# Kernel tuning notes

Measured on AMD Instinct MI355X. Metric: run time of the kernel, lower is better.

Reference implementation:

```python
import jax, jax.numpy as jnp
import numpy as np

B, E, H, L = 16, 64, 8, 2048   # batch, channels(in_channels), heads(node), seq_len
MODES = 64                     # min(modes, L//2) with 'lowest' selection
IDX_Q = np.arange(MODES)       # index_q = sorted(range(modes))
IDX_KV = np.arange(MODES)      # index_kv = sorted(range(modes))


def setup_inputs() -> dict:
    key = jax.random.key(0)
    kq, kk, kv, kr, ki = jax.random.split(key, 5)
    scale = 1.0 / (E * E)  # 1/(in_channels*out_channels)
    return {
        "q": jax.random.normal(kq, (B, E, H, L), jnp.float32),
        "k": jax.random.normal(kk, (B, E, H, L), jnp.float32),
        "v": jax.random.normal(kv, (B, E, H, L), jnp.float32),
        # complex weights1 stored as (real, imag) float parts; torch.rand(cfloat)
        # draws uniform[0,1) real and imag independently, scaled by `scale`.
        "w_re": scale * jax.random.uniform(kr, (H, E, E, MODES), jnp.float32),
        "w_im": scale * jax.random.uniform(ki, (H, E, E, MODES), jnp.float32),
    }


def reference(q, k, v, w_re, w_im):
    # q,k,v: [B,E,H,L] -> [B,H,E,L]; note v is NOT used (matches original module)
    xq = jnp.transpose(q, (0, 2, 1, 3))
    xk = jnp.transpose(k, (0, 2, 1, 3))

    # rFFT along time, gather selected frequency modes: [B,H,E,MODES] complex
    xq_ft_ = jnp.fft.rfft(xq, axis=-1)[..., IDX_Q]
    xk_ft_ = jnp.fft.rfft(xk, axis=-1)[..., IDX_KV]

    # complex cross-attention in mode space: [B,H,MODES,MODES]
    xqk_ft = jnp.einsum('bhex,bhey->bhxy', xq_ft_, xk_ft_)
    xqk_ft = jnp.tanh(xqk_ft)  # complex tanh, matching torch's tensor.tanh()

    # attend over kv modes (values == xk_ft_): [B,H,E,MODES]
    xqkv_ft = jnp.einsum('bhxy,bhey->bhex', xqk_ft, xk_ft_)

    # per-head complex channel mixing: [B,H,E,MODES]
    W = w_re + 1j * w_im  # [H,E,E,MODES]
    xqkvw = jnp.einsum('bhex,heox->bhox', xqkv_ft, W)

    # scatter back into full spectrum and invert
    out_ft = jnp.zeros((B, H, E, L // 2 + 1), jnp.complex64).at[..., IDX_Q].set(xqkvw)
    out = jnp.fft.irfft(out_ft / (E * E), n=L, axis=-1)  # [B,H,E,L] real
    return jnp.transpose(out, (0, 2, 1, 3))  # [B,E,H,L]
```

## Files before the change

kernel.cpp:

```cpp
#include <hip/hip_runtime.h>
#include <math.h>

#define B 16
#define E 64
#define H 8
#define L 2048
#define M 64
#define PLANE (B*H*E*M)

constexpr float CS32[32] = {
     1.0f,                    0.9807852804032304f,   0.9238795325112868f,   0.8314696123025452f,
     0.7071067811865476f,     0.5555702330196022f,   0.3826834323650898f,   0.1950903220161283f,
     0.0f,                   -0.1950903220161283f,  -0.3826834323650898f,  -0.5555702330196022f,
    -0.7071067811865476f,    -0.8314696123025452f,  -0.9238795325112868f,  -0.9807852804032304f,
    -1.0f,                   -0.9807852804032304f,  -0.9238795325112868f,  -0.8314696123025452f,
    -0.7071067811865476f,    -0.5555702330196022f,  -0.3826834323650898f,  -0.1950903220161283f,
     0.0f,                    0.1950903220161283f,   0.3826834323650898f,   0.5555702330196022f,
     0.7071067811865476f,     0.8314696123025452f,   0.9238795325112868f,   0.9807852804032304f
};
constexpr float SN32[32] = {
     0.0f,                    0.1950903220161283f,   0.3826834323650898f,   0.5555702330196022f,
     0.7071067811865476f,     0.8314696123025452f,   0.9238795325112868f,   0.9807852804032304f,
     1.0f,                    0.9807852804032304f,   0.9238795325112868f,   0.8314696123025452f,
     0.7071067811865476f,     0.5555702330196022f,   0.3826834323650898f,   0.1950903220161283f,
     0.0f,                   -0.1950903220161283f,  -0.3826834323650898f,  -0.5555702330196022f,
    -0.7071067811865476f,    -0.8314696123025452f,  -0.9238795325112868f,  -0.9807852804032304f,
    -1.0f,                   -0.9807852804032304f,  -0.9238795325112868f,  -0.8314696123025452f,
    -0.7071067811865476f,    -0.5555702330196022f,  -0.3826834323650898f,  -0.1950903220161283f
};

__device__ inline void ctanhf_stable(float x, float y, float& re, float& im) {
    float ax = fabsf(x);
    if (ax > 11.0f) { re = copysignf(1.0f, x); im = 0.0f; return; }
    float t    = tanf(y);
    float beta = 1.0f + t * t;
    float s    = sinhf(x);
    float rho  = sqrtf(1.0f + s * s);
    float den  = 1.0f + beta * s * s;
    re = (beta * rho * s) / den;
    im = t / den;
}

__global__ __launch_bounds__(256) void k_wtrans(const float* __restrict__ wre,
                                                const float* __restrict__ wim,
                                                float2* __restrict__ Wt,
                                                float2* __restrict__ Tgo,
                                                float2* __restrict__ Cgo)
{
    __shared__ float tre[64][65], tim[64][65];
    int h  = blockIdx.x >> 6, rt = blockIdx.x & 63;
    int tid = threadIdx.x;

    int gidx = blockIdx.x * 256 + tid;
    if (gidx < 2048) {
        int r = gidx >> 6, m = gidx & 63;
        double a = -3.14159265358979323846 * (double)(m * r) / 1024.0;
        Tgo[gidx] = make_float2((float)cos(a), (float)sin(a));
    } else if (gidx < 2080) {
        int j = gidx - 2048;
        double a = -3.14159265358979323846 * (double)j / 32.0;
        Cgo[j] = make_float2((float)cos(a), (float)sin(a));
    }

    int x = tid & 63, r4 = tid >> 6;
    const size_t base = ((size_t)h * 4096 + (size_t)rt * 64) * 64;
    #pragma unroll
    for (int j = 0; j < 16; ++j) {
        int row = j * 4 + r4;
        tre[row][x] = wre[base + (size_t)row * 64 + x];
        tim[row][x] = wim[base + (size_t)row * 64 + x];
    }
    __syncthreads();

    int row = tid & 63, x4 = tid >> 6;
    #pragma unroll
    for (int j = 0; j < 16; ++j) {
        int xx = j * 4 + x4;
        Wt[((size_t)h * 64 + xx) * 4096 + (size_t)rt * 64 + row] =
            make_float2(tre[row][xx], tim[row][xx]);
    }
}

__global__ __launch_bounds__(256) void k_dft(const float* __restrict__ q,
                                             const float* __restrict__ k,
                                             const float2* __restrict__ Tg,
                                             const float2* __restrict__ Cgl,
                                             float2* __restrict__ Xq,
                                             float2* __restrict__ Xk)
{
    __shared__ float2 Ysh[4][64][17];
    __shared__ float2 Tsm[32][64];
    __shared__ float2 Cgs[32];

    int tid  = threadIdx.x;
    int rloc = tid >> 6;
    int lane = tid & 63;
    int rid  = blockIdx.x * 4 + rloc;
    int tensor = rid >> 13;
    int r8 = rid & 8191;
    int b = r8 >> 9, h = (r8 >> 6) & 7, e = r8 & 63;

    #pragma unroll
    for (int j = 0; j < 8; ++j) ((float2*)Tsm)[tid + 256 * j] = Tg[tid + 256 * j];
    if (tid < 32) Cgs[tid] = Cgl[tid];
    __syncthreads();

    const float* src = (tensor ? k : q) + (((size_t)(b * E + e) * H + h) * L) + lane;
    float xs[32];
    #pragma unroll
    for (int i = 0; i < 32; ++i) xs[i] = src[i * 64];

    float s_[16], d_[16];
    #pragma unroll
    for (int i = 1; i <= 15; ++i) { s_[i] = xs[i] + xs[32 - i]; d_[i] = xs[i] - xs[32 - i]; }

    #pragma unroll
    for (int f = 0; f <= 16; ++f) {
        float ar = xs[0] + ((f & 1) ? -xs[16] : xs[16]);
        float ai = 0.f;
        #pragma unroll
        for (int i = 1; i <= 15; ++i) {
            ar = fmaf(s_[i], CS32[(f * i) & 31], ar);
            ai = fmaf(d_[i], SN32[(f * i) & 31], ai);
        }
        Ysh[rloc][lane][f] = make_float2(ar, -ai);
    }

    int mlow = lane & 31;
    int half = lane >> 5;
    int fi   = (mlow <= 16) ? mlow : 32 - mlow;
    float sgn = (mlow <= 16) ? 1.f : -1.f;

    float ar0 = 0.f, ai0 = 0.f, ar1 = 0.f, ai1 = 0.f;
    int rbase = half * 32;
    #pragma unroll
    for (int rb = 0; rb < 4; ++rb) {
        float2 tb[8], t2[8], yb[8];
        #pragma unroll
        for (int j = 0; j < 8; ++j) {
            int rp = rb * 8 + j;
            tb[j] = Tsm[rp][mlow];
            t2[j] = Tsm[rp][mlow + 32];
            yb[j] = Ysh[rloc][rbase + rp][fi];
        }
        #pragma unroll
        for (int j = 0; j < 8; ++j) {
            float yr = yb[j].x, yi = sgn * yb[j].y;
            ar0 = fmaf(yr, tb[j].x, ar0); ar0 = fmaf(-yi, tb[j].y, ar0);
            ai0 = fmaf(yr, tb[j].y, ai0); ai0 = fmaf(yi, tb[j].x, ai0);
            ar1 = fmaf(yr, t2[j].x, ar1); ar1 = fmaf(-yi, t2[j].y, ar1);
            ai1 = fmaf(yr, t2[j].y, ai1); ai1 = fmaf(yi, t2[j].x, ai1);
        }
    }

    if (half) {
        float2 c = Cgs[mlow];
        float t;
        t   = ar0 * c.x - ai0 * c.y;
        ai0 = ar0 * c.y + ai0 * c.x;  ar0 = t;
        t   = ar1 * c.x - ai1 * c.y;
        ai1 = ar1 * c.y + ai1 * c.x;  ar1 = t;
        ar1 = -ar1; ai1 = -ai1;
    }
    ar0 += __shfl_xor(ar0, 32);  ai0 += __shfl_xor(ai0, 32);
    ar1 += __shfl_xor(ar1, 32);  ai1 += __shfl_xor(ai1, 32);

    float2* dst = (tensor ? Xk : Xq) + ((size_t)(b * H + h) * E + e) * M;
    if (!half) dst[mlow]      = make_float2(ar0, ai0);
    else       dst[mlow + 32] = make_float2(ar1, ai1);
}

__global__ __launch_bounds__(256) void k_mid(const float2* __restrict__ Xq,
                                             const float2* __restrict__ Xk,
                                             float2* __restrict__ U)
{
    __shared__ float Qre[64][16], Qim[64][16];
    __shared__ float Kre[64][65], Kim[64][65];

    int bh = blockIdx.x >> 2;
    int xh = (blockIdx.x & 3) * 16;
    int b  = bh >> 3, h = bh & 7;
    int tid = threadIdx.x;
    const float2* xq = Xq + (size_t)bh * 4096;
    const float2* xk = Xk + (size_t)bh * 4096;

    #pragma unroll
    for (int j = 0; j < 4; ++j) {
        int idx = tid + 256 * j;
        int e = idx >> 4, xl = idx & 15;
        float2 v = xq[(e << 6) + xh + xl];
        Qre[e][xl] = v.x; Qim[e][xl] = v.y;
    }
    #pragma unroll
    for (int j = 0; j < 16; ++j) {
        int idx = tid + 256 * j;
        int e = idx >> 6, mm = idx & 63;
        float2 v = xk[idx];
        Kre[e][mm] = v.x; Kim[e][mm] = v.y;
    }
    __syncthreads();

    int x  = tid & 15;
    int y0 = (tid >> 4) * 4;
    float ar[4], ai[4];
    #pragma unroll
    for (int j = 0; j < 4; ++j) { ar[j] = 0.f; ai[j] = 0.f; }

    for (int e = 0; e < 64; ++e) {
        float qr = Qre[e][x], qi = Qim[e][x];
        #pragma unroll
        for (int j = 0; j < 4; ++j) {
            float kr = Kre[e][y0 + j], ki = Kim[e][y0 + j];
            ar[j] = fmaf(qr, kr, ar[j]); ar[j] = fmaf(-qi, ki, ar[j]);
            ai[j] = fmaf(qr, ki, ai[j]); ai[j] = fmaf( qi, kr, ai[j]);
        }
    }
    float trj[4], tij[4];
    #pragma unroll
    for (int j = 0; j < 4; ++j) ctanhf_stable(ar[j], ai[j], trj[j], tij[j]);

    __syncthreads();
    #pragma unroll
    for (int j = 0; j < 4; ++j) { Qre[y0 + j][x] = trj[j]; Qim[y0 + j][x] = tij[j]; }
    __syncthreads();

    int eL    = tid & 63;
    int xslot = tid >> 6;
    float ur[4], ui[4];
    #pragma unroll
    for (int j = 0; j < 4; ++j) { ur[j] = 0.f; ui[j] = 0.f; }

    for (int y = 0; y < 64; ++y) {
        float kr = Kre[eL][y], ki = Kim[eL][y];
        #pragma unroll
        for (int xp = 0; xp < 4; ++xp) {
            int xx = xp * 4 + xslot;
            float sr = Qre[y][xx], si = Qim[y][xx];
            ur[xp] += sr * kr - si * ki;
            ui[xp] += sr * ki + si * kr;
        }
    }
    #pragma unroll
    for (int xp = 0; xp < 4; ++xp) {
        int xx = xp * 4 + xslot;
        U[(((size_t)h * 64 + xh + xx) * 16 + b) * 64 + eL] = make_float2(ur[xp], ui[xp]);
    }
}

__global__ __launch_bounds__(256) void k_wmix(const float2* __restrict__ U,
                                              const float2* __restrict__ Wt,
                                              float2* __restrict__ R)
{
    __shared__ float2 Usm[16][64];
    __shared__ float2 Wsm[64][64];

    int h = blockIdx.x >> 6, x = blockIdx.x & 63;
    int tid = threadIdx.x;

    const float2* usrc = U  + ((size_t)h * 64 + x) * 1024;
    #pragma unroll
    for (int j = 0; j < 4; ++j) {
        int idx = tid + 256 * j;
        ((float2*)Usm)[idx] = usrc[idx];
    }
    const float2* wsrc = Wt + ((size_t)h * 64 + x) * 4096;
    #pragma unroll
    for (int j = 0; j < 16; ++j) {
        int idx = tid + 256 * j;
        ((float2*)Wsm)[idx] = wsrc[idx];
    }
    __syncthreads();

    int o = tid & 63, b0 = tid >> 6;
    float rr[4], ri[4];
    #pragma unroll
    for (int j = 0; j < 4; ++j) { rr[j] = 0.f; ri[j] = 0.f; }

    for (int e = 0; e < 64; ++e) {
        float2 w = Wsm[e][o];
        #pragma unroll
        for (int j = 0; j < 4; ++j) {
            float2 u = Usm[b0 + 4 * j][e];
            rr[j] += u.x * w.x - u.y * w.y;
            ri[j] += u.x * w.y + u.y * w.x;
        }
    }
    #pragma unroll
    for (int j = 0; j < 4; ++j) {
        int b = b0 + 4 * j;
        R[((size_t)(b * H + h) * 64 + o) * 64 + x] = make_float2(rr[j], ri[j]);
    }
}

__global__ __launch_bounds__(256) void k_irfft(const float2* __restrict__ R,
                                               float* __restrict__ out)
{
    __shared__ float2 Fsh[4][64];
    int rloc = threadIdx.x >> 6;
    int r    = threadIdx.x & 63;
    int bho  = blockIdx.x * 4 + rloc;
    int o  = bho & 63, bh = bho >> 6;
    int h  = bh & 7,   b  = bh >> 3;

    Fsh[rloc][r] = R[(size_t)bho * 64 + r];

    float sr_, cr_;
    sincosf(3.0679615757712823e-3f * (float)r, &sr_, &cr_);
    float s32, c32;
    sincosf(9.8174770424681038e-2f * (float)r, &s32, &c32);

    float gr[32], gi[32];
    float wr = 1.f, wi = 0.f;
    #pragma unroll
    for (int f = 0; f < 32; ++f) {
        float2 Fa = Fsh[rloc][f];
        float2 Fb = Fsh[rloc][f + 32];
        float wbr = wr * c32 - wi * s32;
        float wbi = wr * s32 + wi * c32;
        gr[f] = wr * Fa.x - wi * Fa.y + wbr * Fb.x - wbi * Fb.y;
        gi[f] = wr * Fa.y + wi * Fa.x + wbr * Fb.y + wbi * Fb.x;
        float t = wr * cr_ - wi * sr_;
        wi = wr * sr_ + wi * cr_;
        wr = t;
    }
    gr[0] -= 0.5f * Fsh[rloc][0].x;

    const float scl = 2.384185791015625e-7f;
    float* dst = out + ((size_t)(b * E + o) * H + h) * L + r;
    #pragma unroll
    for (int i = 0; i < 16; ++i) {
        float ae = 0.f, ao = 0.f;
        #pragma unroll
        for (int f = 0; f < 32; f += 2) {
            ae = fmaf(gr[f],      CS32[(f * i) & 31],       ae);
            ae = fmaf(gi[f],     -SN32[(f * i) & 31],       ae);
            ao = fmaf(gr[f + 1],  CS32[((f + 1) * i) & 31], ao);
            ao = fmaf(gi[f + 1], -SN32[((f + 1) * i) & 31], ao);
        }
        dst[64 * i]        = scl * (ae + ao);
        dst[64 * (i + 16)] = scl * (ae - ao);
    }
}

extern "C" void kernel_launch(void* const* d_in, const int* in_sizes, int n_in,
                              void* d_out, int out_size, void* d_ws, size_t ws_size,
                              hipStream_t stream)
{
    (void)in_sizes; (void)n_in; (void)out_size; (void)ws_size;
    const float* q    = (const float*)d_in[0];
    const float* k    = (const float*)d_in[1];
    const float* w_re = (const float*)d_in[3];
    const float* w_im = (const float*)d_in[4];
    float* out = (float*)d_out;

    float2* Xq = (float2*)d_out;
    float2* Xk = Xq + PLANE;
    float2* Uu = Xk + PLANE;
    float2* Wt = (float2*)((char*)d_out + (size_t)16 * 1024 * 1024);
    float2* R  = (float2*)d_ws;
    float2* Tg = R + (size_t)PLANE;
    float2* Cg = Tg + 2048;

    k_wtrans<<< 512, 256, 0, stream>>>(w_re, w_im, Wt, Tg, Cg);
    k_dft   <<<4096, 256, 0, stream>>>(q, k, Tg, Cg, Xq, Xk);
    k_mid   <<< 512, 256, 0, stream>>>(Xq, Xk, Uu);
    k_wmix  <<< 512, 256, 0, stream>>>(Uu, Wt, R);
    k_irfft <<<2048, 256, 0, stream>>>(R, out);
}
```

Measured before the change: 95.12 us.

## Halve DFT twiddle table, swizzle split-radix LDS layout, compute twiddles via shuffles

The k_dft kernel now keeps only the first 32 mode columns of the twiddle table in LDS. It derives the upper-half twiddles by multiplying with a per-lane sincosf value broadcast through shuffles, which also replaces the separate Cg table. The intermediate 32-point DFT results are stored as separate real and imaginary floats in an XOR-swizzled layout, intended to cut LDS bank conflicts and footprint. In exchange it adds extra multiplies and shuffles in the inner loop, and the sincosf approximation may slightly change numerics.

```diff
diff --git a/kernel.cpp b/kernel.cpp
--- a/kernel.cpp
+++ b/kernel.cpp
@@ -44,22 +44,17 @@
 __global__ __launch_bounds__(256) void k_wtrans(const float* __restrict__ wre,
                                                 const float* __restrict__ wim,
                                                 float2* __restrict__ Wt,
-                                                float2* __restrict__ Tgo,
-                                                float2* __restrict__ Cgo)
+                                                float2* __restrict__ Tgo)
 {
     __shared__ float tre[64][65], tim[64][65];
     int h  = blockIdx.x >> 6, rt = blockIdx.x & 63;
     int tid = threadIdx.x;
 
     int gidx = blockIdx.x * 256 + tid;
-    if (gidx < 2048) {
-        int r = gidx >> 6, m = gidx & 63;
+    if (gidx < 1024) {
+        int r = gidx >> 5, m = gidx & 31;
         double a = -3.14159265358979323846 * (double)(m * r) / 1024.0;
         Tgo[gidx] = make_float2((float)cos(a), (float)sin(a));
-    } else if (gidx < 2080) {
-        int j = gidx - 2048;
-        double a = -3.14159265358979323846 * (double)j / 32.0;
-        Cgo[j] = make_float2((float)cos(a), (float)sin(a));
     }
 
     int x = tid & 63, r4 = tid >> 6;
@@ -84,13 +79,11 @@
 __global__ __launch_bounds__(256) void k_dft(const float* __restrict__ q,
                                              const float* __restrict__ k,
                                              const float2* __restrict__ Tg,
-                                             const float2* __restrict__ Cgl,
                                              float2* __restrict__ Xq,
                                              float2* __restrict__ Xk)
 {
-    __shared__ float2 Ysh[4][64][17];
-    __shared__ float2 Tsm[32][64];
-    __shared__ float2 Cgs[32];
+    __shared__ float  Smem[4][2048];
+    __shared__ float2 Tsm[32][32];
 
     int tid  = threadIdx.x;
     int rloc = tid >> 6;
@@ -101,9 +94,11 @@
     int b = r8 >> 9, h = (r8 >> 6) & 7, e = r8 & 63;
 
     #pragma unroll
-    for (int j = 0; j < 8; ++j) ((float2*)Tsm)[tid + 256 * j] = Tg[tid + 256 * j];
-    if (tid < 32) Cgs[tid] = Cgl[tid];
-    __syncthreads();
+    for (int j = 0; j < 4; ++j) ((float2*)Tsm)[tid + 256 * j] = Tg[tid + 256 * j];
+    __syncthreads();
+
+    float cgr, cgi;
+    sincosf(-9.8174770424681038e-2f * (float)(lane & 31), &cgi, &cgr);
 
     const float* src = (tensor ? k : q) + (((size_t)(b * E + e) * H + h) * L) + lane;
     float xs[32];
@@ -114,6 +109,8 @@
     #pragma unroll
     for (int i = 1; i <= 15; ++i) { s_[i] = xs[i] + xs[32 - i]; d_[i] = xs[i] - xs[32 - i]; }
 
+    float* Wf = &Smem[rloc][0];
+    int rsw = lane & 31;
     #pragma unroll
     for (int f = 0; f <= 16; ++f) {
         float ar = xs[0] + ((f & 1) ? -xs[16] : xs[16]);
@@ -123,43 +120,50 @@
             ar = fmaf(s_[i], CS32[(f * i) & 31], ar);
             ai = fmaf(d_[i], SN32[(f * i) & 31], ai);
         }
-        Ysh[rloc][lane][f] = make_float2(ar, -ai);
+        Wf[lane * 32 + (f ^ rsw)] = ar;
+        if (f >= 1 && f <= 15) Wf[lane * 32 + ((16 + f) ^ rsw)] = -ai;
     }
 
     int mlow = lane & 31;
     int half = lane >> 5;
     int fi   = (mlow <= 16) ? mlow : 32 - mlow;
     float sgn = (mlow <= 16) ? 1.f : -1.f;
+    int  noim = (fi == 0) | (fi == 16);
+    int  jim  = noim ? 16 : (16 + fi);
+    float imk = noim ? 0.f : sgn;
 
     float ar0 = 0.f, ai0 = 0.f, ar1 = 0.f, ai1 = 0.f;
     int rbase = half * 32;
     #pragma unroll
     for (int rb = 0; rb < 4; ++rb) {
-        float2 tb[8], t2[8], yb[8];
+        float2 tb[8]; float cbr[8], cbi[8], yr[8], yi[8];
         #pragma unroll
         for (int j = 0; j < 8; ++j) {
             int rp = rb * 8 + j;
-            tb[j] = Tsm[rp][mlow];
-            t2[j] = Tsm[rp][mlow + 32];
-            yb[j] = Ysh[rloc][rbase + rp][fi];
+            int r  = rbase + rp;
+            tb[j]  = Tsm[rp][mlow];
+            cbr[j] = __shfl(cgr, rp);
+            cbi[j] = __shfl(cgi, rp);
+            yr[j]  = Wf[r * 32 + (fi ^ rp)];
+            yi[j]  = imk * Wf[r * 32 + (jim ^ rp)];
         }
         #pragma unroll
         for (int j = 0; j < 8; ++j) {
-            float yr = yb[j].x, yi = sgn * yb[j].y;
-            ar0 = fmaf(yr, tb[j].x, ar0); ar0 = fmaf(-yi, tb[j].y, ar0);
-            ai0 = fmaf(yr, tb[j].y, ai0); ai0 = fmaf(yi, tb[j].x, ai0);
-            ar1 = fmaf(yr, t2[j].x, ar1); ar1 = fmaf(-yi, t2[j].y, ar1);
-            ai1 = fmaf(yr, t2[j].y, ai1); ai1 = fmaf(yi, t2[j].x, ai1);
+            ar0 = fmaf(yr[j], tb[j].x, ar0); ar0 = fmaf(-yi[j], tb[j].y, ar0);
+            ai0 = fmaf(yr[j], tb[j].y, ai0); ai0 = fmaf( yi[j], tb[j].x, ai0);
+            float t2r = tb[j].x * cbr[j] - tb[j].y * cbi[j];
+            float t2i = tb[j].x * cbi[j] + tb[j].y * cbr[j];
+            ar1 = fmaf(yr[j], t2r, ar1); ar1 = fmaf(-yi[j], t2i, ar1);
+            ai1 = fmaf(yr[j], t2i, ai1); ai1 = fmaf( yi[j], t2r, ai1);
         }
     }
 
     if (half) {
-        float2 c = Cgs[mlow];
         float t;
-        t   = ar0 * c.x - ai0 * c.y;
-        ai0 = ar0 * c.y + ai0 * c.x;  ar0 = t;
-        t   = ar1 * c.x - ai1 * c.y;
-        ai1 = ar1 * c.y + ai1 * c.x;  ar1 = t;
+        t   = ar0 * cgr - ai0 * cgi;
+        ai0 = ar0 * cgi + ai0 * cgr;  ar0 = t;
+        t   = ar1 * cgr - ai1 * cgi;
+        ai1 = ar1 * cgi + ai1 * cgr;  ar1 = t;
         ar1 = -ar1; ai1 = -ai1;
     }
     ar0 += __shfl_xor(ar0, 32);  ai0 += __shfl_xor(ai0, 32);
@@ -359,10 +363,9 @@
     float2* Wt = (float2*)((char*)d_out + (size_t)16 * 1024 * 1024);
     float2* R  = (float2*)d_ws;
     float2* Tg = R + (size_t)PLANE;
-    float2* Cg = Tg + 2048;
-
-    k_wtrans<<< 512, 256, 0, stream>>>(w_re, w_im, Wt, Tg, Cg);
-    k_dft   <<<4096, 256, 0, stream>>>(q, k, Tg, Cg, Xq, Xk);
+
+    k_wtrans<<< 512, 256, 0, stream>>>(w_re, w_im, Wt, Tg);
+    k_dft   <<<4096, 256, 0, stream>>>(q, k, Tg, Xq, Xk);
     k_mid   <<< 512, 256, 0, stream>>>(Xq, Xk, Uu);
     k_wmix  <<< 512, 256, 0, stream>>>(Uu, Wt, R);
     k_irfft <<<2048, 256, 0, stream>>>(R, out);
```

Measured after the change: 103.1 us. 8.4% more time.
